# Performance work log

Measured on AMD Instinct MI355X. Metric: run time of the kernel, lower is better.

Reference implementation:

```python
import jax, jax.numpy as jnp
from jax import lax
import numpy as np

NB_CODE = 16384
DIM = 128
SCALES = [(1, 1), (2, 2), (4, 4), (8, 8), (16, 16)]
PHI_IDX = [0, 1, 1, 2, 3]  # PhiPartiallyShared: argmin(|ticks - si/(SN-1)|), K=4, SN=5
RESI = 0.5  # abs(quant_resi)
BETA = 0.25


def _cubic(x, a=-0.75):
    # PyTorch bicubic kernel (cubic convolution, a=-0.75)
    ax = np.abs(x)
    return np.where(ax <= 1.0, (a + 2.0) * ax ** 3 - (a + 3.0) * ax ** 2 + 1.0,
                    np.where(ax < 2.0, a * ax ** 3 - 5.0 * a * ax ** 2 + 8.0 * a * ax - 4.0 * a, 0.0))


def bicubic_mat(n_in, n_out):
    # 1D interpolation matrix matching torch F.interpolate(mode='bicubic', align_corners=False)
    W = np.zeros((n_out, n_in), dtype=np.float32)
    scale = n_in / n_out
    for i in range(n_out):
        x = (i + 0.5) * scale - 0.5
        x0 = int(np.floor(x))
        t = x - x0
        for k in range(4):
            idx = min(max(x0 - 1 + k, 0), n_in - 1)  # border clamp
            W[i, idx] += _cubic(t + 1.0 - k)
    return jnp.asarray(W)


def phi_apply(h, w, b):
    y = lax.conv_general_dilated(h, w, (1, 1), 'SAME',
                                 dimension_numbers=('NCHW', 'OIHW', 'NCHW'))
    y = y + b[None, :, None, None]
    return h * (1.0 - RESI) + y * RESI


def setup_inputs() -> dict:
    key = jax.random.key(0)
    k1, k2, k3, k4 = jax.random.split(key, 4)
    B, C, J, L = 16, DIM, 16, 16
    f_bcjl = jax.random.normal(k1, (B, C, J, L), dtype=jnp.float32)
    emb = jax.random.normal(k2, (NB_CODE, C), dtype=jnp.float32) * 0.02
    # 4 partially-shared Phi convs (3x3, C->C)
    phi_w = jax.random.normal(k3, (4, C, C, 3, 3), dtype=jnp.float32) * (1.0 / np.sqrt(C * 9))
    phi_b = jax.random.normal(k4, (4, C), dtype=jnp.float32) * 0.01
    return {'f_bcjl': f_bcjl, 'emb': emb, 'phi_w': phi_w, 'phi_b': phi_b}


def reference(f_bcjl, emb, phi_w, phi_b):
    B, C, J, L = f_bcjl.shape
    SN = len(SCALES)
    f_ng = lax.stop_gradient(f_bcjl)
    f_rest = f_ng
    f_hat = jnp.zeros_like(f_ng)
    loss = jnp.float32(0.0)
    e_sq = jnp.sum(emb * emb, axis=1)  # [K]
    idx_all = []
    for si, (sn, tn) in enumerate(SCALES):
        if si != SN - 1:
            # 'area' downsample == integer-factor average pooling here
            r = f_rest.reshape(B, C, sn, J // sn, tn, L // tn).mean(axis=(3, 5))
        else:
            r = f_rest
        rNC = r.transpose(0, 2, 3, 1).reshape(-1, C)  # [N, C]
        d = jnp.sum(rNC * rNC, axis=1, keepdims=True) + e_sq - 2.0 * (rNC @ emb.T)
        idx = jnp.argmin(d, axis=1)  # [N]
        idx_all.append(idx)
        h = emb[idx].reshape(B, sn, tn, C).transpose(0, 3, 1, 2)  # [B,C,sn,tn]
        if si != SN - 1:
            Wj = bicubic_mat(sn, J)
            Wl = bicubic_mat(tn, L)
            h = jnp.einsum('js,bcst,lt->bcjl', Wj, h, Wl)
        k = PHI_IDX[si]
        h = phi_apply(h, phi_w[k], phi_b[k])
        f_hat = f_hat + h
        f_rest = f_rest - h
        loss = loss + BETA * jnp.mean((lax.stop_gradient(f_hat) - f_bcjl) ** 2) \
                    + jnp.mean((f_hat - f_ng) ** 2)
    loss = loss / SN
    idx_cat = jnp.concatenate(idx_all)
    counts = jnp.zeros((NB_CODE,), jnp.float32).at[idx_cat].add(1.0)
    p = counts / idx_cat.shape[0]
    perplexity = jnp.exp(-jnp.sum(p * jnp.log(p + 1e-10)))
    # straight-through estimator
    f_hat_out = lax.stop_gradient(f_hat) - f_ng + f_bcjl
    return (f_hat_out, loss, perplexity)
```

## Files before the change

kernel.cpp:

```cpp
#include <hip/hip_runtime.h>
#include <hip/hip_bf16.h>
#include <math.h>

#define BATCH 16
#define CDIM  128
#define NCODE 16384
#define ELEMS 524288
#define NTOT  5456
#define WEXT_TOT 589824
#define LOSS_COEF 4.76837158203125e-7f

typedef __attribute__((ext_vector_type(8))) short short8;
typedef __attribute__((ext_vector_type(4))) float float4v;
typedef unsigned short ushortT;
typedef unsigned long long u64;
typedef unsigned int u32;

__device__ __forceinline__ ushortT f2bf(float x) {
    __hip_bfloat16 h = __float2bfloat16(x);
    return *reinterpret_cast<ushortT*>(&h);
}
__device__ __forceinline__ float bf2f(ushortT b) {
    __hip_bfloat16 h = *reinterpret_cast<__hip_bfloat16*>(&b);
    return __bfloat162float(h);
}
__device__ __forceinline__ u32 ford(float v) {
    u32 b = __float_as_uint(v);
    return b ^ ((u32)((int)b >> 31) | 0x80000000u);
}

__device__ double cubic_d(double x) {
    const double a = -0.75;
    double ax = fabs(x);
    if (ax <= 1.0) return (a + 2.0) * ax * ax * ax - (a + 3.0) * ax * ax + 1.0;
    if (ax < 2.0)  return a * ax * ax * ax - 5.0 * a * ax * ax + 8.0 * a * ax - 4.0 * a;
    return 0.0;
}

__global__ __launch_bounds__(256)
void k_prologue(const float* __restrict__ f, const float* __restrict__ emb,
                const float* __restrict__ phi_w,
                float* __restrict__ f_rest, float* __restrict__ f_hat,
                float* __restrict__ esq, ushortT* __restrict__ embext,
                ushortT* __restrict__ wext, float* __restrict__ wmat,
                float* __restrict__ lossA) {
    const int t = threadIdx.x;
    const int id = blockIdx.x * 256 + t;

    if (id < ELEMS) {
        f_rest[id] = f[id];
        f_hat[id] = 0.f;
        int row = id >> 5, c4 = id & 31;
        float4 v = reinterpret_cast<const float4*>(emb + (size_t)row * CDIM)[c4];
        float xs[4] = {v.x, v.y, v.z, v.w};
        ushortT hi[4], lo[4];
        float ss = 0.f;
        #pragma unroll
        for (int i = 0; i < 4; ++i) {
            hi[i] = f2bf(xs[i]);
            lo[i] = f2bf(xs[i] - bf2f(hi[i]));
            ss += xs[i] * xs[i];
        }
        ushortT* base = embext + (size_t)row * 256;
        *reinterpret_cast<ushort4*>(base + c4 * 4)       = make_ushort4(hi[0], hi[1], hi[2], hi[3]);
        *reinterpret_cast<ushort4*>(base + 128 + c4 * 4) = make_ushort4(lo[0], lo[1], lo[2], lo[3]);
        #pragma unroll
        for (int off = 16; off; off >>= 1) ss += __shfl_down(ss, off);
        if ((t & 31) == 0) esq[row] = ss;
    }
    if (id < WEXT_TOT) {
        int k4 = id / 147456, rem = id % 147456;
        int co = rem / 1152, kk = rem % 1152;
        int off = kk >> 7, ci = kk & 127;
        float v = 0.5f * phi_w[(((size_t)(k4 * 128 + co)) * 128 + ci) * 9 + off];
        if (ci == co && off == 4) v += 0.5f;
        wext[id] = f2bf(v);
    }
    if (blockIdx.x == 0 && t < 64) {
        int sIdx = t >> 4;
        int S = 1 << sIdx;
        int j = t & 15;
        const int offs[4] = {0, 16, 48, 112};
        double row[8];
        for (int s = 0; s < 8; ++s) row[s] = 0.0;
        double scale = (double)S / 16.0;
        double x = (j + 0.5) * scale - 0.5;
        double x0 = floor(x);
        double tt = x - x0;
        for (int k = 0; k < 4; ++k) {
            int idx = (int)x0 - 1 + k;
            idx = idx < 0 ? 0 : (idx > S - 1 ? S - 1 : idx);
            row[idx] += cubic_d(tt + 1.0 - k);
        }
        for (int s = 0; s < S; ++s) wmat[offs[sIdx] + j * S + s] = (float)row[s];
    }
    if (id == 0) lossA[0] = 0.f;
}

__global__ __launch_bounds__(256)
void k_packext(const float* __restrict__ fr, ushortT* __restrict__ re,
               u64* __restrict__ packed, int N, int padN, int S, int lgS) {
    int id = blockIdx.x * 256 + threadIdx.x;
    if (id < N) packed[id] = ~0ull;
    if (id >= padN * 32) return;
    int row = id >> 5, c4 = id & 31;
    ushortT hi[4], lo[4];
    if (row < N) {
        int mask = S - 1;
        int tt = row & mask, ssi = (row >> lgS) & mask, b = row >> (2 * lgS);
        int bs = 16 >> lgS;
        float inv = 1.f / (float)(bs * bs);
        #pragma unroll
        for (int u = 0; u < 4; ++u) {
            int c = c4 * 4 + u;
            const float* base = fr + (size_t)(b * 128 + c) * 256 + (ssi * bs) * 16 + tt * bs;
            float acc = 0.f;
            for (int jj = 0; jj < bs; ++jj)
                for (int ll = 0; ll < bs; ++ll)
                    acc += base[jj * 16 + ll];
            float x = acc * inv;
            hi[u] = f2bf(x);
            lo[u] = f2bf(x - bf2f(hi[u]));
        }
    } else {
        #pragma unroll
        for (int u = 0; u < 4; ++u) { hi[u] = 0; lo[u] = 0; }
    }
    ushortT* base = re + (size_t)row * 256;
    *reinterpret_cast<ushort4*>(base + c4 * 4)       = make_ushort4(hi[0], hi[1], hi[2], hi[3]);
    *reinterpret_cast<ushort4*>(base + 128 + c4 * 4) = make_ushort4(lo[0], lo[1], lo[2], lo[3]);
}

__global__ __launch_bounds__(256)
void k_packext_wave(const float* __restrict__ fr, ushortT* __restrict__ re,
                    u64* __restrict__ packed, int N, int padN, int S, int lgS) {
    int gid = blockIdx.x * 256 + threadIdx.x;
    int wid = gid >> 6, lane = threadIdx.x & 63;
    if (wid >= padN * 128) return;
    int row = wid >> 7, c = wid & 127;
    float x = 0.f;
    if (row < N) {
        int mask = S - 1;
        int tt = row & mask, ssi = (row >> lgS) & mask, b = row >> (2 * lgS);
        int lgbs = 4 - lgS, bs = 1 << lgbs, cnt = bs * bs;
        const float* base = fr + (size_t)(b * 128 + c) * 256 + (ssi * bs) * 16 + tt * bs;
        float acc = 0.f;
        for (int e = lane; e < cnt; e += 64)
            acc += base[(e >> lgbs) * 16 + (e & (bs - 1))];
        #pragma unroll
        for (int off = 32; off; off >>= 1) acc += __shfl_down(acc, off);
        x = acc / (float)cnt;
    }
    if (lane == 0) {
        ushortT h = f2bf(x);
        re[(size_t)row * 256 + c] = h;
        re[(size_t)row * 256 + 128 + c] = f2bf(x - bf2f(h));
        if (c == 0 && row < N) packed[row] = ~0ull;
    }
}

__global__ __launch_bounds__(256)
void k_argmin_mfma(const ushortT* __restrict__ rext, const ushortT* __restrict__ embext,
                   const float* __restrict__ esq, int N, int kPerSplit,
                   u64* __restrict__ packed) {
    __shared__ ushortT Btile[2][64 * 32 * 8];
    const int t = threadIdx.x;
    const int w = t >> 6;
    const int lane = t & 63;
    const int ln = lane & 15;
    const int q  = lane >> 4;
    const int k0beg = blockIdx.y * kPerSplit;
    const int rowW = blockIdx.x * 128 + w * 32;

    short8 a[2][8];
    #pragma unroll
    for (int ti = 0; ti < 2; ++ti) {
        const ushortT* r0 = rext + (size_t)(rowW + ti * 16 + ln) * 256 + q * 8;
        #pragma unroll
        for (int sb = 0; sb < 8; ++sb)
            a[ti][sb] = *reinterpret_cast<const short8*>(r0 + sb * 32);
    }

    float minv[2][4];
    int   mini[2][4];
    #pragma unroll
    for (int ti = 0; ti < 2; ++ti)
        #pragma unroll
        for (int rg = 0; rg < 4; ++rg) { minv[ti][rg] = 3.4e38f; mini[ti][rg] = 0; }

    const int tiles = kPerSplit >> 6;

    #pragma unroll
    for (int i = 0; i < 8; ++i) {
        int F = (i * 4 + w) * 64 + lane;
        int n = F >> 5, cs = F & 31;
        int cp = (cs & ~7) | ((cs & 7) ^ (n & 7));
        const ushortT* src = embext + (size_t)(k0beg + n) * 256 + cp * 8;
        __builtin_amdgcn_global_load_lds(
            (const __attribute__((address_space(1))) unsigned int*)src,
            (__attribute__((address_space(3))) unsigned int*)&Btile[0][(size_t)((i * 4 + w) * 64) * 8],
            16, 0, 0);
    }

    for (int it = 0; it < tiles; ++it) {
        __syncthreads();
        if (it + 1 < tiles) {
            int k1 = k0beg + (it + 1) * 64;
            int bu = (it + 1) & 1;
            #pragma unroll
            for (int i = 0; i < 8; ++i) {
                int F = (i * 4 + w) * 64 + lane;
                int n = F >> 5, cs = F & 31;
                int cp = (cs & ~7) | ((cs & 7) ^ (n & 7));
                const ushortT* src = embext + (size_t)(k1 + n) * 256 + cp * 8;
                __builtin_amdgcn_global_load_lds(
                    (const __attribute__((address_space(1))) unsigned int*)src,
                    (__attribute__((address_space(3))) unsigned int*)&Btile[bu][(size_t)((i * 4 + w) * 64) * 8],
                    16, 0, 0);
            }
        }
        const ushortT* Bt = Btile[it & 1];
        const int k0 = k0beg + it * 64;

        #pragma unroll
        for (int sub = 0; sub < 4; ++sub) {
            int n = sub * 16 + ln;
            short8 bfr[8];
            #pragma unroll
            for (int sb = 0; sb < 8; ++sb) {
                int cp = q + 4 * sb;
                int cs = (cp & ~7) | ((cp & 7) ^ (n & 7));
                bfr[sb] = *reinterpret_cast<const short8*>(&Bt[(size_t)(n * 32 + cs) * 8]);
            }
            float4v acc[2];
            #pragma unroll
            for (int ti = 0; ti < 2; ++ti) acc[ti] = (float4v){0.f, 0.f, 0.f, 0.f};
            #pragma unroll
            for (int s = 0; s < 12; ++s) {
                int as = s < 8 ? s : s - 8;
                int bs = s < 4 ? s : s - 4;
                #pragma unroll
                for (int ti = 0; ti < 2; ++ti)
                    acc[ti] = __builtin_amdgcn_mfma_f32_16x16x32_bf16(a[ti][as], bfr[bs], acc[ti], 0, 0, 0);
            }
            int kc = k0 + sub * 16 + ln;
            float es = esq[kc];
            #pragma unroll
            for (int ti = 0; ti < 2; ++ti)
                #pragma unroll
                for (int rg = 0; rg < 4; ++rg) {
                    float sc = fmaf(-2.f, acc[ti][rg], es);
                    if (sc < minv[ti][rg]) { minv[ti][rg] = sc; mini[ti][rg] = kc; }
                }
        }
    }

    #pragma unroll
    for (int ti = 0; ti < 2; ++ti)
        #pragma unroll
        for (int rg = 0; rg < 4; ++rg) {
            float v = minv[ti][rg]; int ix = mini[ti][rg];
            #pragma unroll
            for (int off = 1; off < 16; off <<= 1) {
                float ov = __shfl_xor(v, off);
                int   oi = __shfl_xor(ix, off);
                if (ov < v || (ov == v && oi < ix)) { v = ov; ix = oi; }
            }
            if (ln == 0) {
                int row = rowW + ti * 16 + q * 4 + rg;
                if (row < N) {
                    u64 p = ((u64)ford(v) << 32) | (u32)ix;
                    atomicMin(&packed[row], p);
                }
            }
        }
}

__global__ __launch_bounds__(256)
void k_upconv(const float* __restrict__ emb, const u64* __restrict__ packed,
              const float* __restrict__ wm, int S, int lastScale,
              const ushortT* __restrict__ wext, const float* __restrict__ bias,
              const float* __restrict__ f_in, float* __restrict__ f_hat,
              float* __restrict__ f_rest, float* __restrict__ loss_acc) {
    __shared__ __align__(16) ushortT Htile[3 * 16 * 128];
    __shared__ __align__(16) float tmpS[3 * 8 * 128];
    __shared__ float wsum[4];
    const int t = threadIdx.x;
    const int b = blockIdx.x >> 4;
    const int j = blockIdx.x & 15;
    const int l = t >> 4, c8 = t & 15;
    const int phys = (c8 & 8) | ((c8 & 7) ^ (l & 7));

    if (lastScale) {
        #pragma unroll
        for (int r = 0; r < 3; ++r) {
            int jin = j - 1 + r;
            float acc[8] = {0.f, 0.f, 0.f, 0.f, 0.f, 0.f, 0.f, 0.f};
            if (jin >= 0 && jin < 16) {
                int idx = (int)(u32)(packed[(b * 16 + jin) * 16 + l] & 0xFFFFFFFFull);
                const float* er = emb + (size_t)idx * CDIM + c8 * 8;
                float4 e0 = *reinterpret_cast<const float4*>(er);
                float4 e1 = *reinterpret_cast<const float4*>(er + 4);
                acc[0] = e0.x; acc[1] = e0.y; acc[2] = e0.z; acc[3] = e0.w;
                acc[4] = e1.x; acc[5] = e1.y; acc[6] = e1.z; acc[7] = e1.w;
            }
            short8 o;
            #pragma unroll
            for (int i = 0; i < 8; ++i) o[i] = (short)f2bf(acc[i]);
            *reinterpret_cast<short8*>(&Htile[((size_t)(r * 16 + l) * 16 + phys) * 8]) = o;
        }
    } else {
        int items = 3 * S * 16;
        for (int i = t; i < items; i += 256) {
            int r = i / (S * 16);
            int rem = i - r * (S * 16);
            int t2 = rem >> 4, cc8 = rem & 15;
            int jin = j - 1 + r;
            float a0[8] = {0.f, 0.f, 0.f, 0.f, 0.f, 0.f, 0.f, 0.f};
            if (jin >= 0 && jin < 16) {
                for (int s = 0; s < S; ++s) {
                    float wjv = wm[jin * S + s];
                    int idx = (int)(u32)(packed[b * S * S + s * S + t2] & 0xFFFFFFFFull);
                    const float* er = emb + (size_t)idx * CDIM + cc8 * 8;
                    float4 e0 = *reinterpret_cast<const float4*>(er);
                    float4 e1 = *reinterpret_cast<const float4*>(er + 4);
                    a0[0] += wjv * e0.x; a0[1] += wjv * e0.y;
                    a0[2] += wjv * e0.z; a0[3] += wjv * e0.w;
                    a0[4] += wjv * e1.x; a0[5] += wjv * e1.y;
                    a0[6] += wjv * e1.z; a0[7] += wjv * e1.w;
                }
            }
            float* tp = &tmpS[((size_t)(r * 8 + t2)) * 128 + cc8 * 8];
            *reinterpret_cast<float4*>(tp)     = make_float4(a0[0], a0[1], a0[2], a0[3]);
            *reinterpret_cast<float4*>(tp + 4) = make_float4(a0[4], a0[5], a0[6], a0[7]);
        }
        __syncthreads();
        #pragma unroll
        for (int r = 0; r < 3; ++r) {
            float acc[8] = {0.f, 0.f, 0.f, 0.f, 0.f, 0.f, 0.f, 0.f};
            for (int t2 = 0; t2 < S; ++t2) {
                float wlv = wm[l * S + t2];
                const float* tp = &tmpS[((size_t)(r * 8 + t2)) * 128 + c8 * 8];
                float4 v0 = *reinterpret_cast<const float4*>(tp);
                float4 v1 = *reinterpret_cast<const float4*>(tp + 4);
                acc[0] += wlv * v0.x; acc[1] += wlv * v0.y;
                acc[2] += wlv * v0.z; acc[3] += wlv * v0.w;
                acc[4] += wlv * v1.x; acc[5] += wlv * v1.y;
                acc[6] += wlv * v1.z; acc[7] += wlv * v1.w;
            }
            short8 o;
            #pragma unroll
            for (int i = 0; i < 8; ++i) o[i] = (short)f2bf(acc[i]);
            *reinterpret_cast<short8*>(&Htile[((size_t)(r * 16 + l) * 16 + phys) * 8]) = o;
        }
    }
    __syncthreads();

    const int w = t >> 6, lane = t & 63;
    const int ln = lane & 15, q = lane >> 4;
    const int co0 = w * 32;
    const ushortT* wA = wext + (size_t)(co0 + ln) * 1152;
    float4v acc2[2] = {{0.f, 0.f, 0.f, 0.f}, {0.f, 0.f, 0.f, 0.f}};
    const short8 zz = {0, 0, 0, 0, 0, 0, 0, 0};

    #pragma unroll 3
    for (int off = 0; off < 9; ++off) {
        const int dj = off / 3, dl = off % 3;
        int cIn = ln + dl - 1;
        int cCl = cIn < 0 ? 0 : (cIn > 15 ? 15 : cIn);
        bool oob = (cIn != cCl);
        int rb = (dj * 16 + cCl) * 128;
        #pragma unroll
        for (int g = 0; g < 4; ++g) {
            int csl = g * 4 + q;
            int ph2 = (csl & 8) | ((csl & 7) ^ (cCl & 7));
            short8 av = *reinterpret_cast<const short8*>(&Htile[rb + ph2 * 8]);
            if (oob) av = zz;
            const ushortT* wr = wA + (off * 4 + g) * 32 + q * 8;
            short8 b0 = *reinterpret_cast<const short8*>(wr);
            short8 b1 = *reinterpret_cast<const short8*>(wr + 16 * 1152);
            acc2[0] = __builtin_amdgcn_mfma_f32_16x16x32_bf16(av, b0, acc2[0], 0, 0, 0);
            acc2[1] = __builtin_amdgcn_mfma_f32_16x16x32_bf16(av, b1, acc2[1], 0, 0, 0);
        }
    }

    float s = 0.f;
    #pragma unroll
    for (int sn = 0; sn < 2; ++sn) {
        int co = co0 + sn * 16 + ln;
        float bsv = 0.5f * bias[co];
        size_t gi = ((size_t)(b * 128 + co) * 16 + j) * 16 + q * 4;
        float4 fh = *reinterpret_cast<const float4*>(&f_hat[gi]);
        float4 fr = *reinterpret_cast<const float4*>(&f_rest[gi]);
        float4 fv = *reinterpret_cast<const float4*>(&f_in[gi]);
        float o0 = acc2[sn][0] + bsv, o1 = acc2[sn][1] + bsv;
        float o2 = acc2[sn][2] + bsv, o3 = acc2[sn][3] + bsv;
        fh.x += o0; fh.y += o1; fh.z += o2; fh.w += o3;
        fr.x -= o0; fr.y -= o1; fr.z -= o2; fr.w -= o3;
        *reinterpret_cast<float4*>(&f_hat[gi]) = fh;
        *reinterpret_cast<float4*>(&f_rest[gi]) = fr;
        float d0 = fh.x - fv.x, d1 = fh.y - fv.y;
        float d2 = fh.z - fv.z, d3 = fh.w - fv.w;
        s += d0 * d0 + d1 * d1 + d2 * d2 + d3 * d3;
    }
    #pragma unroll
    for (int off = 32; off; off >>= 1) s += __shfl_down(s, off);
    if (lane == 0) wsum[w] = s;
    __syncthreads();
    if (t == 0)
        atomicAdd(loss_acc, (wsum[0] + wsum[1] + wsum[2] + wsum[3]) * LOSS_COEF);
}

__global__ __launch_bounds__(256)
void k_final(const u64* __restrict__ packed, const float* __restrict__ loss_acc,
             float* __restrict__ out) {
    __shared__ u32 cnt2[NCODE / 2];
    __shared__ float ws4[4];
    int t = threadIdx.x;
    for (int i = t; i < NCODE / 2; i += 256) cnt2[i] = 0;
    __syncthreads();
    for (int i = t; i < NTOT; i += 256) {
        int idx = (int)(u32)(packed[i] & 0xFFFFFFFFull);
        atomicAdd(&cnt2[idx >> 1], (idx & 1) ? 65536u : 1u);
    }
    __syncthreads();
    float s = 0.f;
    for (int k = t; k < NCODE; k += 256) {
        u32 c = cnt2[k >> 1];
        c = (k & 1) ? (c >> 16) : (c & 0xFFFFu);
        float p = (float)c * (1.0f / (float)NTOT);
        s += p * logf(p + 1e-10f);
    }
    #pragma unroll
    for (int off = 32; off; off >>= 1) s += __shfl_down(s, off);
    if ((t & 63) == 0) ws4[t >> 6] = s;
    __syncthreads();
    if (t == 0) {
        out[ELEMS]     = loss_acc[0];
        out[ELEMS + 1] = expf(-(ws4[0] + ws4[1] + ws4[2] + ws4[3]));
    }
}

extern "C" void kernel_launch(void* const* d_in, const int* in_sizes, int n_in,
                              void* d_out, int out_size, void* d_ws, size_t ws_size,
                              hipStream_t stream) {
    const float* f     = (const float*)d_in[0];
    const float* emb   = (const float*)d_in[1];
    const float* phi_w = (const float*)d_in[2];
    const float* phi_b = (const float*)d_in[3];
    float* out = (float*)d_out;

    float* wsf = (float*)d_ws;
    float*   f_rest = wsf;
    float*   esq    = wsf + 524288;
    float*   wmat   = wsf + 540672;
    float*   lossA  = wsf + 540928;
    u64*     packed = (u64*)(wsf + 540992);
    ushortT* embext = (ushortT*)(wsf + 557376);
    ushortT* rext   = (ushortT*)(wsf + 2654528);
    ushortT* wext   = (ushortT*)(wsf + 3178816);

    k_prologue<<<2304, 256, 0, stream>>>(f, emb, phi_w, f_rest, out, esq,
                                         embext, wext, wmat, lossA);

    const int Ss[5]     = {1, 2, 4, 8, 16};
    const int lgSs[5]   = {0, 1, 2, 3, 4};
    const int phiIdx[5] = {0, 1, 1, 2, 3};
    const int ksplit[5] = {256, 256, 128, 64, 16};
    const int wmOff[5]  = {0, 16, 48, 112, 0};
    const int pOff[5]   = {0, 16, 80, 336, 1360};

    for (int si = 0; si < 5; ++si) {
        int S = Ss[si], lgS = lgSs[si];
        int N = 16 * S * S;
        int padN = (N + 127) & ~127;
        u64* pk = packed + pOff[si];

        if (S <= 2)
            k_packext_wave<<<padN * 128 / 4, 256, 0, stream>>>(f_rest, rext, pk, N, padN, S, lgS);
        else
            k_packext<<<padN * 32 / 256, 256, 0, stream>>>(f_rest, rext, pk, N, padN, S, lgS);

        int KS = ksplit[si];
        k_argmin_mfma<<<dim3(padN / 128, KS), 256, 0, stream>>>(rext, embext, esq,
                                                                N, NCODE / KS, pk);

        int k = phiIdx[si];
        k_upconv<<<256, 256, 0, stream>>>(emb, pk, wmat + wmOff[si], S, si == 4 ? 1 : 0,
                                          wext + (size_t)k * 147456,
                                          phi_b + (size_t)k * 128, f, out, f_rest, lossA);
    }

    k_final<<<1, 256, 0, stream>>>(packed, lossA, out);
}
```

Before: 326.4 us.

## Fold scale packing into prologue and upconv epilogue, drop redundant packext launches

The first-scale mean pooling and bf16 hi/lo packing move into the prologue, and the final full-resolution packing is written directly from the upconv epilogue of scale 3. This removes two packext launches, and the last f_rest write-back, which nothing reads afterwards, is skipped. Initialising the packed argmin buffer moves to the prologue, and the argmin grid becomes 1-D with row and split indices decoded from blockIdx.x. The trade-off is scattered 2-byte stores from the upconv epilogue, plus extra branching and a block-level reduction in the prologue.

```diff
diff --git a/kernel.cpp b/kernel.cpp
--- a/kernel.cpp
+++ b/kernel.cpp
@@ -43,12 +43,16 @@
                 float* __restrict__ f_rest, float* __restrict__ f_hat,
                 float* __restrict__ esq, ushortT* __restrict__ embext,
                 ushortT* __restrict__ wext, float* __restrict__ wmat,
-                float* __restrict__ lossA) {
+                float* __restrict__ lossA, ushortT* __restrict__ rext,
+                u64* __restrict__ packed) {
+    __shared__ float red[4];
     const int t = threadIdx.x;
-    const int id = blockIdx.x * 256 + t;
-
-    if (id < ELEMS) {
-        f_rest[id] = f[id];
+    const int bid = blockIdx.x;
+    const int id = bid * 256 + t;
+
+    if (bid < 2048) {
+        float fv = f[id];
+        f_rest[id] = fv;
         f_hat[id] = 0.f;
         int row = id >> 5, c4 = id & 31;
         float4 v = reinterpret_cast<const float4*>(emb + (size_t)row * CDIM)[c4];
@@ -67,6 +71,23 @@
         #pragma unroll
         for (int off = 16; off; off >>= 1) ss += __shfl_down(ss, off);
         if ((t & 31) == 0) esq[row] = ss;
+
+        float s = fv;
+        #pragma unroll
+        for (int off = 32; off; off >>= 1) s += __shfl_down(s, off);
+        if ((t & 63) == 0) red[t >> 6] = s;
+        __syncthreads();
+        if (t == 0) {
+            float m = (red[0] + red[1] + red[2] + red[3]) * (1.f / 256.f);
+            int b = bid >> 7, c = bid & 127;
+            ushortT h = f2bf(m);
+            rext[b * 256 + c] = h;
+            rext[b * 256 + 128 + c] = f2bf(m - bf2f(h));
+        }
+    } else {
+        int idz = (bid - 2048) * 256 + t;
+        if (idz < 30720)
+            reinterpret_cast<u32*>(rext + 16 * 256)[idz] = 0;
     }
     if (id < WEXT_TOT) {
         int k4 = id / 147456, rem = id % 147456;
@@ -76,7 +97,7 @@
         if (ci == co && off == 4) v += 0.5f;
         wext[id] = f2bf(v);
     }
-    if (blockIdx.x == 0 && t < 64) {
+    if (bid == 0 && t < 64) {
         int sIdx = t >> 4;
         int S = 1 << sIdx;
         int j = t & 15;
@@ -95,13 +116,13 @@
         for (int s = 0; s < S; ++s) wmat[offs[sIdx] + j * S + s] = (float)row[s];
     }
     if (id == 0) lossA[0] = 0.f;
+    if (id < 8192) packed[id] = ~0ull;
 }
 
 __global__ __launch_bounds__(256)
 void k_packext(const float* __restrict__ fr, ushortT* __restrict__ re,
-               u64* __restrict__ packed, int N, int padN, int S, int lgS) {
+               int N, int padN, int S, int lgS) {
     int id = blockIdx.x * 256 + threadIdx.x;
-    if (id < N) packed[id] = ~0ull;
     if (id >= padN * 32) return;
     int row = id >> 5, c4 = id & 31;
     ushortT hi[4], lo[4];
@@ -133,7 +154,7 @@
 
 __global__ __launch_bounds__(256)
 void k_packext_wave(const float* __restrict__ fr, ushortT* __restrict__ re,
-                    u64* __restrict__ packed, int N, int padN, int S, int lgS) {
+                    int N, int padN, int S, int lgS) {
     int gid = blockIdx.x * 256 + threadIdx.x;
     int wid = gid >> 6, lane = threadIdx.x & 63;
     if (wid >= padN * 128) return;
@@ -155,13 +176,12 @@
         ushortT h = f2bf(x);
         re[(size_t)row * 256 + c] = h;
         re[(size_t)row * 256 + 128 + c] = f2bf(x - bf2f(h));
-        if (c == 0 && row < N) packed[row] = ~0ull;
     }
 }
 
 __global__ __launch_bounds__(256)
 void k_argmin_mfma(const ushortT* __restrict__ rext, const ushortT* __restrict__ embext,
-                   const float* __restrict__ esq, int N, int kPerSplit,
+                   const float* __restrict__ esq, int N, int kPerSplit, int KS,
                    u64* __restrict__ packed) {
     __shared__ ushortT Btile[2][64 * 32 * 8];
     const int t = threadIdx.x;
@@ -169,8 +189,11 @@
     const int lane = t & 63;
     const int ln = lane & 15;
     const int q  = lane >> 4;
-    const int k0beg = blockIdx.y * kPerSplit;
-    const int rowW = blockIdx.x * 128 + w * 32;
+    const int bid = blockIdx.x;
+    const int ky = bid % KS;
+    const int rb = bid / KS;
+    const int k0beg = ky * kPerSplit;
+    const int rowW = rb * 128 + w * 32;
 
     short8 a[2][8];
     #pragma unroll
@@ -281,7 +304,8 @@
               const float* __restrict__ wm, int S, int lastScale,
               const ushortT* __restrict__ wext, const float* __restrict__ bias,
               const float* __restrict__ f_in, float* __restrict__ f_hat,
-              float* __restrict__ f_rest, float* __restrict__ loss_acc) {
+              float* __restrict__ f_rest, float* __restrict__ loss_acc,
+              int storeRest, int packNext, ushortT* __restrict__ rext_out) {
     __shared__ __align__(16) ushortT Htile[3 * 16 * 128];
     __shared__ __align__(16) float tmpS[3 * 8 * 128];
     __shared__ float wsum[4];
@@ -391,17 +415,34 @@
         float bsv = 0.5f * bias[co];
         size_t gi = ((size_t)(b * 128 + co) * 16 + j) * 16 + q * 4;
         float4 fh = *reinterpret_cast<const float4*>(&f_hat[gi]);
-        float4 fr = *reinterpret_cast<const float4*>(&f_rest[gi]);
         float4 fv = *reinterpret_cast<const float4*>(&f_in[gi]);
-        float o0 = acc2[sn][0] + bsv, o1 = acc2[sn][1] + bsv;
-        float o2 = acc2[sn][2] + bsv, o3 = acc2[sn][3] + bsv;
-        fh.x += o0; fh.y += o1; fh.z += o2; fh.w += o3;
-        fr.x -= o0; fr.y -= o1; fr.z -= o2; fr.w -= o3;
-        *reinterpret_cast<float4*>(&f_hat[gi]) = fh;
-        *reinterpret_cast<float4*>(&f_rest[gi]) = fr;
-        float d0 = fh.x - fv.x, d1 = fh.y - fv.y;
-        float d2 = fh.z - fv.z, d3 = fh.w - fv.w;
-        s += d0 * d0 + d1 * d1 + d2 * d2 + d3 * d3;
+        float oo[4] = {acc2[sn][0] + bsv, acc2[sn][1] + bsv,
+                       acc2[sn][2] + bsv, acc2[sn][3] + bsv};
+        float fhv[4] = {fh.x + oo[0], fh.y + oo[1], fh.z + oo[2], fh.w + oo[3]};
+        *reinterpret_cast<float4*>(&f_hat[gi]) =
+            make_float4(fhv[0], fhv[1], fhv[2], fhv[3]);
+        float fvv[4] = {fv.x, fv.y, fv.z, fv.w};
+        #pragma unroll
+        for (int i = 0; i < 4; ++i) {
+            float d = fhv[i] - fvv[i];
+            s += d * d;
+        }
+        if (storeRest || packNext) {
+            float4 fr = *reinterpret_cast<const float4*>(&f_rest[gi]);
+            float frn[4] = {fr.x - oo[0], fr.y - oo[1], fr.z - oo[2], fr.w - oo[3]};
+            if (storeRest)
+                *reinterpret_cast<float4*>(&f_rest[gi]) =
+                    make_float4(frn[0], frn[1], frn[2], frn[3]);
+            if (packNext) {
+                #pragma unroll
+                for (int i = 0; i < 4; ++i) {
+                    int row = b * 256 + j * 16 + q * 4 + i;
+                    ushortT hv = f2bf(frn[i]);
+                    rext_out[(size_t)row * 256 + co] = hv;
+                    rext_out[(size_t)row * 256 + 128 + co] = f2bf(frn[i] - bf2f(hv));
+                }
+            }
+        }
     }
     #pragma unroll
     for (int off = 32; off; off >>= 1) s += __shfl_down(s, off);
@@ -461,7 +502,7 @@
     ushortT* wext   = (ushortT*)(wsf + 3178816);
 
     k_prologue<<<2304, 256, 0, stream>>>(f, emb, phi_w, f_rest, out, esq,
-                                         embext, wext, wmat, lossA);
+                                         embext, wext, wmat, lossA, rext, packed);
 
     const int Ss[5]     = {1, 2, 4, 8, 16};
     const int lgSs[5]   = {0, 1, 2, 3, 4};
@@ -476,19 +517,20 @@
         int padN = (N + 127) & ~127;
         u64* pk = packed + pOff[si];
 
-        if (S <= 2)
-            k_packext_wave<<<padN * 128 / 4, 256, 0, stream>>>(f_rest, rext, pk, N, padN, S, lgS);
-        else
-            k_packext<<<padN * 32 / 256, 256, 0, stream>>>(f_rest, rext, pk, N, padN, S, lgS);
+        if (si == 1)
+            k_packext_wave<<<padN * 128 / 4, 256, 0, stream>>>(f_rest, rext, N, padN, S, lgS);
+        else if (si == 2 || si == 3)
+            k_packext<<<padN * 32 / 256, 256, 0, stream>>>(f_rest, rext, N, padN, S, lgS);
 
         int KS = ksplit[si];
-        k_argmin_mfma<<<dim3(padN / 128, KS), 256, 0, stream>>>(rext, embext, esq,
-                                                                N, NCODE / KS, pk);
+        k_argmin_mfma<<<(padN / 128) * KS, 256, 0, stream>>>(rext, embext, esq,
+                                                             N, NCODE / KS, KS, pk);
 
         int k = phiIdx[si];
         k_upconv<<<256, 256, 0, stream>>>(emb, pk, wmat + wmOff[si], S, si == 4 ? 1 : 0,
                                           wext + (size_t)k * 147456,
-                                          phi_b + (size_t)k * 128, f, out, f_rest, lossA);
+                                          phi_b + (size_t)k * 128, f, out, f_rest, lossA,
+                                          si <= 2 ? 1 : 0, si == 3 ? 1 : 0, rext);
     }
 
     k_final<<<1, 256, 0, stream>>>(packed, lossA, out);
```

After: 320.2 us (median of 2 runs). Within noise of the previous version (-1.9%).
